# Kernel tuning notes

Hardware: AMD Instinct MI355X
Metric: run time of the kernel (lower is better)

## Reference

```python
import jax, jax.numpy as jnp
import numpy as np

B, T, F = 4096, 72, 9
H = 64            # GRU units per direction
DENSE = 128
P = 24            # predict_window


def _gru_scan(xp, h0, U, br, act):
    """xp: (T,B,3H) precomputed input projections; Keras reset_after=True GRU."""
    def step(h, x_t):
        rec = h @ U + br                      # (B,3H)
        xz, xr, xh = jnp.split(x_t, 3, axis=-1)
        rz, rr, rh = jnp.split(rec, 3, axis=-1)
        z = jax.nn.sigmoid(xz + rz)
        r = jax.nn.sigmoid(xr + rr)
        hh = act(xh + r * rh)
        h_new = z * h + (1.0 - z) * hh
        return h_new, h_new
    hT, hs = jax.lax.scan(step, h0, xp)
    return hT, hs


def _bigru(x, h0f, h0b, Wf, Uf, bif, brf, Wb, Ub, bib, brb, act, return_sequences):
    xt = jnp.swapaxes(x, 0, 1)                # (T,B,F)
    xpf = xt @ Wf + bif                       # (T,B,3H)
    xpb = xt[::-1] @ Wb + bib                 # reversed time for backward dir
    hTf, hsf = _gru_scan(xpf, h0f, Uf, brf, act)
    hTb, hsb = _gru_scan(xpb, h0b, Ub, brb, act)
    if return_sequences:
        out = jnp.concatenate([hsf, hsb[::-1]], axis=-1)   # (T,B,2H)
        return jnp.swapaxes(out, 0, 1)                      # (B,T,2H)
    return jnp.concatenate([hTf, hTb], axis=-1)             # (B,2H)


def _glorot(key, shape):
    fan_in, fan_out = shape[0], shape[-1]
    lim = np.sqrt(6.0 / (fan_in + fan_out))
    return jax.random.uniform(key, shape, jnp.float32, -lim, lim)


def setup_inputs() -> dict:
    key = jax.random.key(0)
    ks = jax.random.split(key, 16)
    d = {
        "x": jax.random.normal(ks[0], (B, T, F), jnp.float32),
        "h0_fwd": jnp.zeros((B, H), jnp.float32),
        "h0_bwd": jnp.zeros((B, H), jnp.float32),
        # d1 (input F=9), forward & backward directions
        "d1f_W": _glorot(ks[1], (F, 3 * H)), "d1f_U": _glorot(ks[2], (H, 3 * H)),
        "d1f_bi": jnp.zeros((3 * H,), jnp.float32), "d1f_br": jnp.zeros((3 * H,), jnp.float32),
        "d1b_W": _glorot(ks[3], (F, 3 * H)), "d1b_U": _glorot(ks[4], (H, 3 * H)),
        "d1b_bi": jnp.zeros((3 * H,), jnp.float32), "d1b_br": jnp.zeros((3 * H,), jnp.float32),
        # d2 (input 2H=128)
        "d2f_W": _glorot(ks[5], (2 * H, 3 * H)), "d2f_U": _glorot(ks[6], (H, 3 * H)),
        "d2f_bi": jnp.zeros((3 * H,), jnp.float32), "d2f_br": jnp.zeros((3 * H,), jnp.float32),
        "d2b_W": _glorot(ks[7], (2 * H, 3 * H)), "d2b_U": _glorot(ks[8], (H, 3 * H)),
        "d2b_bi": jnp.zeros((3 * H,), jnp.float32), "d2b_br": jnp.zeros((3 * H,), jnp.float32),
        # dense heads
        "dense_W": _glorot(ks[9], (2 * H, DENSE)), "dense_b": jnp.zeros((DENSE,), jnp.float32),
        "out_W": _glorot(ks[10], (DENSE, P)), "out_b": jnp.zeros((P,), jnp.float32),
    }
    return d


def reference(x, h0_fwd, h0_bwd,
              d1f_W, d1f_U, d1f_bi, d1f_br, d1b_W, d1b_U, d1b_bi, d1b_br,
              d2f_W, d2f_U, d2f_bi, d2f_br, d2b_W, d2b_U, d2b_bi, d2b_br,
              dense_W, dense_b, out_W, out_b):
    # d1: Bidirectional GRU(64, activation=relu), return_sequences=True, initial_state=hidden
    seq = _bigru(x, h0_fwd, h0_bwd,
                 d1f_W, d1f_U, d1f_bi, d1f_br,
                 d1b_W, d1b_U, d1b_bi, d1b_br,
                 jax.nn.relu, True)                         # (B,T,128)
    # d2: Bidirectional GRU(64, activation=tanh), zero initial state, last-state output
    z0 = jnp.zeros((x.shape[0], H), seq.dtype)
    feat = _bigru(seq, z0, z0,
                  d2f_W, d2f_U, d2f_bi, d2f_br,
                  d2b_W, d2b_U, d2b_bi, d2b_br,
                  jnp.tanh, False)                          # (B,128)
    h = jax.nn.relu(feat @ dense_W + dense_b)               # (B,128)
    out = jax.nn.softmax(h @ out_W + out_b, axis=-1)        # (B,P)
    return out
```

## Files before the change

### kernel.cpp

```cpp
#include <hip/hip_runtime.h>
#include <hip/hip_bf16.h>

typedef __attribute__((ext_vector_type(8))) short short8;
typedef __attribute__((ext_vector_type(4))) float f32x4;

#define MFMA_B16(a, b, c) __builtin_amdgcn_mfma_f32_16x16x32_bf16((a), (b), (c), 0, 0, 0)

__device__ __forceinline__ float bf2f(unsigned short u) {
    union { unsigned int i; float f; } v; v.i = ((unsigned int)u) << 16; return v.f;
}
__device__ __forceinline__ unsigned short f2bf(float f) {
    union { float f; unsigned int i; } v; v.f = f;
    unsigned int r = v.i + 0x7fffu + ((v.i >> 16) & 1u);
    return (unsigned short)(r >> 16);
}
__device__ __forceinline__ float rcp_f(float x) { return __builtin_amdgcn_rcpf(x); }
__device__ __forceinline__ float sigm_pre(float x) {
    return rcp_f(1.0f + __builtin_amdgcn_exp2f(x));
}
__device__ __forceinline__ float tanh_pre(float x) {
    return 1.0f - 2.0f * rcp_f(__builtin_amdgcn_exp2f(x) + 1.0f);
}

__device__ __forceinline__ bool probe_bf16(const unsigned short* p, int tid, int* s_cnt) {
    if (tid == 0) *s_cnt = 0;
    __syncthreads();
    unsigned short s = p[tid & 255];
    int e = (s >> 7) & 0xFF;
    if (tid < 256 && e >= 117 && e <= 137) atomicAdd(s_cnt, 1);
    __syncthreads();
    return *s_cnt >= 200;
}

struct WArgs {
    const void* src[20];
    int off[21];
};

__global__ __launch_bounds__(256)
void convert_w(WArgs a, unsigned short* __restrict__ arena,
               const unsigned short* __restrict__ probe)
{
    __shared__ int cnt;
    const bool bf = probe_bf16(probe, threadIdx.x, &cnt);
    const int total = a.off[20];
    for (int i = blockIdx.x * 256 + threadIdx.x; i < total; i += gridDim.x * 256) {
        int t = 0;
        while (t < 19 && i >= a.off[t + 1]) ++t;
        const int local = i - a.off[t];
        float v = bf ? bf2f(((const unsigned short*)a.src[t])[local])
                     : ((const float*)a.src[t])[local];
        if (t < 16) {
            const int col = local % 192;
            if (col < 128) v *= -1.4426950408889634f;
            else if (t >= 8) v *= 2.885390081777927f;
        }
        arena[i] = f2bf(v);
    }
}

__global__ __launch_bounds__(256, 1)
void gru1_kernel(const void* __restrict__ X, const void* __restrict__ h0f,
                 const void* __restrict__ h0b, int cb, int bchunk,
                 const unsigned short* __restrict__ Wf, const unsigned short* __restrict__ Uf,
                 const unsigned short* __restrict__ bif, const unsigned short* __restrict__ brf,
                 const unsigned short* __restrict__ Wb, const unsigned short* __restrict__ Ub,
                 const unsigned short* __restrict__ bib, const unsigned short* __restrict__ brb,
                 unsigned short* __restrict__ seq)
{
    const int tid  = threadIdx.x;
    const int lane = tid & 63;
    const int wv   = tid >> 6;
    const int q    = lane >> 4;
    const int ln   = lane & 15;
    const int dir  = blockIdx.y;
    const int lb0  = blockIdx.x * 16;
    const int gb0  = cb + lb0;
    const int u    = wv * 16 + ln;

    const unsigned short* W  = dir ? Wb  : Wf;
    const unsigned short* U  = dir ? Ub  : Uf;
    const unsigned short* bi = dir ? bib : bif;
    const unsigned short* br = dir ? brb : brf;
    const void* h0 = dir ? h0b : h0f;

    __shared__ __align__(16) unsigned short Ah[2][16][72];
    __shared__ __align__(16) unsigned short Ax[2][16][40];
    __shared__ int s_cnt;

    const bool xbf = probe_bf16((const unsigned short*)X, tid, &s_cnt);

    {
        unsigned short* p = &Ax[0][0][0];
        for (int i = tid; i < 2 * 16 * 40; i += 256) p[i] = 0;
    }
    __syncthreads();

    {
        const int tx0 = dir ? 71 : 0;
        if (tid < 144) {
            int r = tid / 9, k = tid - 9 * r;
            size_t idx = ((size_t)(gb0 + r) * 72 + tx0) * 9 + k;
            unsigned short hv, lv;
            if (xbf) { hv = ((const unsigned short*)X)[idx]; lv = 0; }
            else { float v = ((const float*)X)[idx]; hv = f2bf(v); lv = f2bf(v - bf2f(hv)); }
            Ax[0][r][2 * k]     = hv;
            Ax[0][r][2 * k + 1] = lv;
        }
    }

    short8 bU[3][2];
    short8 bW[3];
#pragma unroll
    for (int g = 0; g < 3; ++g) {
        const int col = g * 64 + u;
#pragma unroll
        for (int ks = 0; ks < 2; ++ks) {
            short8 f;
#pragma unroll
            for (int j = 0; j < 8; ++j) {
                int kp = ks * 32 + q * 8 + j;
                f[j] = (short)U[(size_t)kp * 192 + col];
            }
            bU[g][ks] = f;
        }
        short8 fw;
#pragma unroll
        for (int j = 0; j < 8; ++j) {
            int kp = q * 8 + j;
            fw[j] = (kp < 18) ? (short)W[(size_t)(kp >> 1) * 192 + col] : (short)0;
        }
        bW[g] = fw;
    }

    const float bz  = bf2f(bi[u])       + bf2f(br[u]);
    const float brg = bf2f(bi[64 + u])  + bf2f(br[64 + u]);
    const float bih = bf2f(bi[128 + u]);
    const float brh = bf2f(br[128 + u]);
    const f32x4 Cz  = {bz,  bz,  bz,  bz};
    const f32x4 Cr  = {brg, brg, brg, brg};
    const f32x4 Chx = {bih, bih, bih, bih};
    const f32x4 Chr = {brh, brh, brh, brh};

    float hreg[4];
#pragma unroll
    for (int i = 0; i < 4; ++i) {
        int m = q * 4 + i;
        size_t idx = (size_t)(gb0 + m) * 64 + u;
        float hv = xbf ? bf2f(((const unsigned short*)h0)[idx])
                       : ((const float*)h0)[idx];
        hreg[i] = hv;
        Ah[0][m][u] = f2bf(hv);
    }

    const int r2 = tid >> 3, c2 = tid & 7;
    const int r0x = tid / 9, k0x = tid - 9 * r0x;

    unsigned short ch = 0, cl = 0;
    if (tid < 144) {
        const int tx = dir ? 70 : 1;
        size_t idx = ((size_t)(gb0 + r0x) * 72 + tx) * 9 + k0x;
        if (xbf) { ch = ((const unsigned short*)X)[idx]; cl = 0; }
        else { float v = ((const float*)X)[idx]; ch = f2bf(v); cl = f2bf(v - bf2f(ch)); }
    }
    __syncthreads();

#pragma unroll 2
    for (int t = 0; t < 72; ++t) {
        const int cur = t & 1, nb = cur ^ 1;

        unsigned short fh = 0, fl = 0;
        if (t < 70 && tid < 144) {
            const int tx = dir ? (69 - t) : (t + 2);
            size_t idx = ((size_t)(gb0 + r0x) * 72 + tx) * 9 + k0x;
            if (xbf) { fh = ((const unsigned short*)X)[idx]; fl = 0; }
            else { float v = ((const float*)X)[idx]; fh = f2bf(v); fl = f2bf(v - bf2f(fh)); }
        }

        if (t > 0 && tid < 128) {
            const int tw = dir ? (71 - (t - 1)) : (t - 1);
            int4 v = *(const int4*)&Ah[cur][r2][c2 * 8];
            *(int4*)(seq + ((size_t)tw * bchunk + lb0 + r2) * 128 + dir * 64 + c2 * 8) = v;
        }

        const unsigned short* ap = &Ah[cur][ln][0];
        short8 a0 = *(const short8*)(ap + q * 8);
        short8 a1 = *(const short8*)(ap + 32 + q * 8);
        short8 ax = *(const short8*)(&Ax[cur][ln][q * 8]);
        f32x4 az  = MFMA_B16(ax, bW[0], Cz);
        az        = MFMA_B16(a0, bU[0][0], az);
        az        = MFMA_B16(a1, bU[0][1], az);
        f32x4 ar  = MFMA_B16(ax, bW[1], Cr);
        ar        = MFMA_B16(a0, bU[1][0], ar);
        ar        = MFMA_B16(a1, bU[1][1], ar);
        f32x4 ahx = MFMA_B16(ax, bW[2], Chx);
        f32x4 ahr = MFMA_B16(a0, bU[2][0], Chr);
        ahr       = MFMA_B16(a1, bU[2][1], ahr);

#pragma unroll
        for (int i = 0; i < 4; ++i) {
            const int m = q * 4 + i;
            float z = sigm_pre(az[i]);
            float r = sigm_pre(ar[i]);
            float pre = ahx[i] + r * ahr[i];
            float hh = fmaxf(pre, 0.0f);
            float hn = hh + z * (hreg[i] - hh);
            hreg[i] = hn;
            Ah[nb][m][u] = f2bf(hn);
        }

        if (t < 71 && tid < 144) {
            Ax[nb][r0x][2 * k0x]     = ch;
            Ax[nb][r0x][2 * k0x + 1] = cl;
        }
        ch = fh; cl = fl;
        __syncthreads();
    }

    if (tid < 128) {
        const int tw = dir ? 0 : 71;
        int4 v = *(const int4*)&Ah[0][r2][c2 * 8];
        *(int4*)(seq + ((size_t)tw * bchunk + lb0 + r2) * 128 + dir * 64 + c2 * 8) = v;
    }
}

__global__ __launch_bounds__(256, 1)
void gru2_kernel(const unsigned short* __restrict__ seq, int cb, int bchunk,
                 const unsigned short* __restrict__ W2f, const unsigned short* __restrict__ U2f,
                 const unsigned short* __restrict__ bi2f, const unsigned short* __restrict__ br2f,
                 const unsigned short* __restrict__ W2b, const unsigned short* __restrict__ U2b,
                 const unsigned short* __restrict__ bi2b, const unsigned short* __restrict__ br2b,
                 float* __restrict__ feat)
{
    const int tid  = threadIdx.x;
    const int lane = tid & 63;
    const int wv   = tid >> 6;
    const int q    = lane >> 4;
    const int ln   = lane & 15;
    const int dir  = blockIdx.y;
    const int lb0  = blockIdx.x * 16;
    const int gb0  = cb + lb0;
    const int u    = wv * 16 + ln;

    const unsigned short* W  = dir ? W2b  : W2f;
    const unsigned short* U  = dir ? U2b  : U2f;
    const unsigned short* bi = dir ? bi2b : bi2f;
    const unsigned short* br = dir ? br2b : br2f;

    __shared__ __align__(16) unsigned short Ah[2][16][72];

    {
        unsigned short* p = &Ah[0][0][0];
        for (int i = tid; i < 16 * 72; i += 256) p[i] = 0;
    }

    const long long tstride = (long long)bchunk * 128 * (dir ? -1 : 1);
    const unsigned short* sptr0 = seq + ((size_t)(lb0 + ln)) * 128 + q * 8
                                + (dir ? 71ll * bchunk * 128 : 0);

    short8 bU[3][2];
    short8 bV[3][4];
#pragma unroll
    for (int g = 0; g < 3; ++g) {
        const int col = g * 64 + u;
#pragma unroll
        for (int ks = 0; ks < 2; ++ks) {
            short8 f;
#pragma unroll
            for (int j = 0; j < 8; ++j) {
                int kp = ks * 32 + q * 8 + j;
                f[j] = (short)U[(size_t)kp * 192 + col];
            }
            bU[g][ks] = f;
        }
#pragma unroll
        for (int ks = 0; ks < 4; ++ks) {
            short8 fv;
#pragma unroll
            for (int j = 0; j < 8; ++j) {
                int kp = ks * 32 + q * 8 + j;
                fv[j] = (short)W[(size_t)kp * 192 + col];
            }
            bV[g][ks] = fv;
        }
    }

    const float bz  = bf2f(bi[u])       + bf2f(br[u]);
    const float brg = bf2f(bi[64 + u])  + bf2f(br[64 + u]);
    const float bih = bf2f(bi[128 + u]);
    const float brh = bf2f(br[128 + u]);
    const f32x4 Cz  = {bz,  bz,  bz,  bz};
    const f32x4 Cr  = {brg, brg, brg, brg};
    const f32x4 Chx = {bih, bih, bih, bih};
    const f32x4 Chr = {brh, brh, brh, brh};

    float hreg[4];
#pragma unroll
    for (int i = 0; i < 4; ++i) hreg[i] = 0.0f;

    f32x4 P0, P1, P2;
    {
        const unsigned short* sp = sptr0;
        short8 s0 = *(const short8*)(sp);
        short8 s1 = *(const short8*)(sp + 32);
        short8 s2 = *(const short8*)(sp + 64);
        short8 s3 = *(const short8*)(sp + 96);
        P0 = MFMA_B16(s0, bV[0][0], Cz);
        P0 = MFMA_B16(s1, bV[0][1], P0);
        P0 = MFMA_B16(s2, bV[0][2], P0);
        P0 = MFMA_B16(s3, bV[0][3], P0);
        P1 = MFMA_B16(s0, bV[1][0], Cr);
        P1 = MFMA_B16(s1, bV[1][1], P1);
        P1 = MFMA_B16(s2, bV[1][2], P1);
        P1 = MFMA_B16(s3, bV[1][3], P1);
        P2 = MFMA_B16(s0, bV[2][0], Chx);
        P2 = MFMA_B16(s1, bV[2][1], P2);
        P2 = MFMA_B16(s2, bV[2][2], P2);
        P2 = MFMA_B16(s3, bV[2][3], P2);
    }
    short8 c0, c1, c2, c3;
    {
        const unsigned short* sp = sptr0 + tstride;
        c0 = *(const short8*)(sp);
        c1 = *(const short8*)(sp + 32);
        c2 = *(const short8*)(sp + 64);
        c3 = *(const short8*)(sp + 96);
    }
    __syncthreads();

#pragma unroll 2
    for (int t = 0; t < 72; ++t) {
        const int cur = t & 1, nb = cur ^ 1;

        short8 f0, f1, f2, f3;
        const bool pf2 = (t < 70);
        if (pf2) {
            const unsigned short* sp = sptr0 + (long long)(t + 2) * tstride;
            f0 = *(const short8*)(sp);
            f1 = *(const short8*)(sp + 32);
            f2 = *(const short8*)(sp + 64);
            f3 = *(const short8*)(sp + 96);
        }

        const unsigned short* ap = &Ah[cur][ln][0];
        short8 a0 = *(const short8*)(ap + q * 8);
        short8 a1 = *(const short8*)(ap + 32 + q * 8);
        f32x4 az  = MFMA_B16(a0, bU[0][0], P0);
        az        = MFMA_B16(a1, bU[0][1], az);
        f32x4 ar  = MFMA_B16(a0, bU[1][0], P1);
        ar        = MFMA_B16(a1, bU[1][1], ar);
        f32x4 ahr = MFMA_B16(a0, bU[2][0], Chr);
        ahr       = MFMA_B16(a1, bU[2][1], ahr);
        f32x4 ahx = P2;

#pragma unroll
        for (int i = 0; i < 4; ++i) {
            const int m = q * 4 + i;
            float z = sigm_pre(az[i]);
            float r = sigm_pre(ar[i]);
            float pre = ahx[i] + r * ahr[i];
            float hh = tanh_pre(pre);
            float hn = hh + z * (hreg[i] - hh);
            hreg[i] = hn;
            Ah[nb][m][u] = f2bf(hn);
        }

        if (t < 71) {
            P0 = MFMA_B16(c0, bV[0][0], Cz);
            P0 = MFMA_B16(c1, bV[0][1], P0);
            P0 = MFMA_B16(c2, bV[0][2], P0);
            P0 = MFMA_B16(c3, bV[0][3], P0);
            P1 = MFMA_B16(c0, bV[1][0], Cr);
            P1 = MFMA_B16(c1, bV[1][1], P1);
            P1 = MFMA_B16(c2, bV[1][2], P1);
            P1 = MFMA_B16(c3, bV[1][3], P1);
            P2 = MFMA_B16(c0, bV[2][0], Chx);
            P2 = MFMA_B16(c1, bV[2][1], P2);
            P2 = MFMA_B16(c2, bV[2][2], P2);
            P2 = MFMA_B16(c3, bV[2][3], P2);
        }
        if (pf2) { c0 = f0; c1 = f1; c2 = f2; c3 = f3; }
        __syncthreads();
    }

#pragma unroll
    for (int i = 0; i < 4; ++i) {
        const int m = q * 4 + i;
        feat[(size_t)(gb0 + m) * 128 + dir * 64 + u] = hreg[i];
    }
}

__global__ __launch_bounds__(256, 1)
void head_kernel(const float* __restrict__ feat,
                 const unsigned short* __restrict__ dW, const unsigned short* __restrict__ db,
                 const unsigned short* __restrict__ oW, const unsigned short* __restrict__ ob,
                 float* __restrict__ out)
{
    const int tid = threadIdx.x;
    const int b0  = blockIdx.x * 16;

    __shared__ __align__(16) unsigned short Wl[128][136];
    __shared__ __align__(16) float fs[16][128];
    __shared__ __align__(16) float hs[16][136];
    __shared__ __align__(16) float ls[16][32];

    for (int i = tid; i < 2048; i += 256) {
        const int k = i >> 4;
        const int c = (i & 15) * 8;
        *(int4*)&Wl[k][c] = *(const int4*)(dW + (size_t)k * 128 + c);
    }
    {
        const float4* src = (const float4*)(feat + (size_t)b0 * 128);
        float4* dst = (float4*)&fs[0][0];
        for (int i = tid; i < 512; i += 256) dst[i] = src[i];
    }
    __syncthreads();

    {
        const int row = tid >> 4;
        const int j0  = (tid & 15) * 8;
        float acc[8];
#pragma unroll
        for (int jj = 0; jj < 8; ++jj) acc[jj] = bf2f(db[j0 + jj]);
        for (int k = 0; k < 128; ++k) {
            float f = fs[row][k];
            short8 w = *(const short8*)&Wl[k][j0];
#pragma unroll
            for (int jj = 0; jj < 8; ++jj)
                acc[jj] += f * bf2f((unsigned short)w[jj]);
        }
#pragma unroll
        for (int jj = 0; jj < 8; ++jj) hs[row][j0 + jj] = fmaxf(acc[jj], 0.0f);
    }
    __syncthreads();

    for (int e = tid; e < 16 * 24; e += 256) {
        const int row = e / 24, l = e - 24 * row;
        float acc = bf2f(ob[l]);
        for (int k = 0; k < 128; ++k)
            acc += hs[row][k] * bf2f(oW[(size_t)k * 24 + l]);
        ls[row][l] = acc;
    }
    __syncthreads();

    for (int e = tid; e < 16 * 24; e += 256) {
        const int row = e / 24, l = e - 24 * row;
        float mx = ls[row][0];
#pragma unroll
        for (int k = 1; k < 24; ++k) mx = fmaxf(mx, ls[row][k]);
        float s = 0.0f;
#pragma unroll
        for (int k = 0; k < 24; ++k) s += __expf(ls[row][k] - mx);
        float v = __expf(ls[row][l] - mx) * rcp_f(s);
        out[(size_t)(b0 + row) * 24 + l] = v;
    }
}

extern "C" void kernel_launch(void* const* d_in, const int* in_sizes, int n_in,
                              void* d_out, int out_size, void* d_ws, size_t ws_size,
                              hipStream_t stream) {
    (void)in_sizes; (void)n_in; (void)out_size;

    static const int wc[20] = {
        1728, 12288, 192, 192,
        1728, 12288, 192, 192,
        24576, 12288, 192, 192,
        24576, 12288, 192, 192,
        16384, 128,
        3072, 24
    };

    WArgs a;
    int off = 0;
    for (int t = 0; t < 20; ++t) {
        a.src[t] = d_in[t + 3];
        a.off[t] = off;
        off += wc[t];
    }
    a.off[20] = off;

    const unsigned long long arena_bytes = 245952ull;
    const unsigned long long feat_bytes  = 4096ull * 128ull * 4ull;
    const unsigned long long seq_full    = 72ull * 4096ull * 128ull * 2ull;
    const unsigned long long fixed       = arena_bytes + feat_bytes;

    int nc = 32;
    for (int c = 1; c <= 32; c *= 2) {
        if (fixed + seq_full / (unsigned long long)c <= (unsigned long long)ws_size) { nc = c; break; }
    }
    const int bchunk = 4096 / nc;

    unsigned short* arena = (unsigned short*)d_ws;
    float* feat           = (float*)((char*)d_ws + arena_bytes);
    unsigned short* seq   = (unsigned short*)((char*)d_ws + fixed);

    convert_w<<<128, 256, 0, stream>>>(a, arena, (const unsigned short*)d_in[0]);

    const unsigned short* d1fW = arena + a.off[0];
    const unsigned short* d1fU = arena + a.off[1];
    const unsigned short* d1fbi= arena + a.off[2];
    const unsigned short* d1fbr= arena + a.off[3];
    const unsigned short* d1bW = arena + a.off[4];
    const unsigned short* d1bU = arena + a.off[5];
    const unsigned short* d1bbi= arena + a.off[6];
    const unsigned short* d1bbr= arena + a.off[7];
    const unsigned short* d2fW = arena + a.off[8];
    const unsigned short* d2fU = arena + a.off[9];
    const unsigned short* d2fbi= arena + a.off[10];
    const unsigned short* d2fbr= arena + a.off[11];
    const unsigned short* d2bW = arena + a.off[12];
    const unsigned short* d2bU = arena + a.off[13];
    const unsigned short* d2bbi= arena + a.off[14];
    const unsigned short* d2bbr= arena + a.off[15];
    const unsigned short* dW   = arena + a.off[16];
    const unsigned short* db   = arena + a.off[17];
    const unsigned short* oW   = arena + a.off[18];
    const unsigned short* ob   = arena + a.off[19];

    for (int c = 0; c < nc; ++c) {
        const int cb = c * bchunk;
        gru1_kernel<<<dim3(bchunk / 16, 2), 256, 0, stream>>>(
            d_in[0], d_in[1], d_in[2], cb, bchunk,
            d1fW, d1fU, d1fbi, d1fbr, d1bW, d1bU, d1bbi, d1bbr, seq);
        gru2_kernel<<<dim3(bchunk / 16, 2), 256, 0, stream>>>(
            seq, cb, bchunk,
            d2fW, d2fU, d2fbi, d2fbr, d2bW, d2bU, d2bbi, d2bbr, feat);
    }
    head_kernel<<<256, 256, 0, stream>>>(
        feat, dW, db, oW, ob, (float*)d_out);
}
```

Measured before the change: 255.4 us.

## Process two 16-row batch tiles per block in both GRU kernels

Each block of both GRU recurrence kernels now handles 32 batch rows as two independent 16-row MFMA tiles instead of one, and the grid is halved to match. The two tiles' MFMA chains and gate math are interleaved so one wave has independent work to hide MFMA and transcendental latency in the serial time loop. Weight fragments held in registers and the per-step barrier are shared across both tiles. In exchange there are fewer blocks, which may leave CUs idle, plus more registers per wave and double the LDS footprint.

```diff
diff --git a/kernel.cpp b/kernel.cpp
--- a/kernel.cpp
+++ b/kernel.cpp
@@ -74,7 +74,7 @@
     const int q    = lane >> 4;
     const int ln   = lane & 15;
     const int dir  = blockIdx.y;
-    const int lb0  = blockIdx.x * 16;
+    const int lb0  = blockIdx.x * 32;
     const int gb0  = cb + lb0;
     const int u    = wv * 16 + ln;
 
@@ -84,22 +84,22 @@
     const unsigned short* br = dir ? brb : brf;
     const void* h0 = dir ? h0b : h0f;
 
-    __shared__ __align__(16) unsigned short Ah[2][16][72];
-    __shared__ __align__(16) unsigned short Ax[2][16][40];
+    __shared__ __align__(16) unsigned short Ah[2][32][72];
+    __shared__ __align__(16) unsigned short Ax[2][32][40];
     __shared__ int s_cnt;
 
     const bool xbf = probe_bf16((const unsigned short*)X, tid, &s_cnt);
 
     {
         unsigned short* p = &Ax[0][0][0];
-        for (int i = tid; i < 2 * 16 * 40; i += 256) p[i] = 0;
+        for (int i = tid; i < 2 * 32 * 40; i += 256) p[i] = 0;
     }
     __syncthreads();
 
     {
         const int tx0 = dir ? 71 : 0;
-        if (tid < 144) {
-            int r = tid / 9, k = tid - 9 * r;
+        for (int i = tid; i < 288; i += 256) {
+            int r = i / 9, k = i - 9 * r;
             size_t idx = ((size_t)(gb0 + r) * 72 + tx0) * 9 + k;
             unsigned short hv, lv;
             if (xbf) { hv = ((const unsigned short*)X)[idx]; lv = 0; }
@@ -142,26 +142,35 @@
     const f32x4 Chx = {bih, bih, bih, bih};
     const f32x4 Chr = {brh, brh, brh, brh};
 
-    float hreg[4];
+    float hA[4], hB[4];
 #pragma unroll
     for (int i = 0; i < 4; ++i) {
         int m = q * 4 + i;
-        size_t idx = (size_t)(gb0 + m) * 64 + u;
-        float hv = xbf ? bf2f(((const unsigned short*)h0)[idx])
-                       : ((const float*)h0)[idx];
-        hreg[i] = hv;
-        Ah[0][m][u] = f2bf(hv);
+        size_t ia = (size_t)(gb0 + m) * 64 + u;
+        size_t ib = (size_t)(gb0 + 16 + m) * 64 + u;
+        float va = xbf ? bf2f(((const unsigned short*)h0)[ia]) : ((const float*)h0)[ia];
+        float vb = xbf ? bf2f(((const unsigned short*)h0)[ib]) : ((const float*)h0)[ib];
+        hA[i] = va; hB[i] = vb;
+        Ah[0][m][u]      = f2bf(va);
+        Ah[0][16 + m][u] = f2bf(vb);
     }
 
     const int r2 = tid >> 3, c2 = tid & 7;
     const int r0x = tid / 9, k0x = tid - 9 * r0x;
-
-    unsigned short ch = 0, cl = 0;
-    if (tid < 144) {
+    const int i1  = 256 + tid;
+    const int r1x = i1 / 9, k1x = i1 - 9 * r1x;
+
+    unsigned short ch0 = 0, cl0 = 0, ch1 = 0, cl1 = 0;
+    {
         const int tx = dir ? 70 : 1;
         size_t idx = ((size_t)(gb0 + r0x) * 72 + tx) * 9 + k0x;
-        if (xbf) { ch = ((const unsigned short*)X)[idx]; cl = 0; }
-        else { float v = ((const float*)X)[idx]; ch = f2bf(v); cl = f2bf(v - bf2f(ch)); }
+        if (xbf) { ch0 = ((const unsigned short*)X)[idx]; cl0 = 0; }
+        else { float v = ((const float*)X)[idx]; ch0 = f2bf(v); cl0 = f2bf(v - bf2f(ch0)); }
+        if (tid < 32) {
+            size_t idx1 = ((size_t)(gb0 + r1x) * 72 + tx) * 9 + k1x;
+            if (xbf) { ch1 = ((const unsigned short*)X)[idx1]; cl1 = 0; }
+            else { float v = ((const float*)X)[idx1]; ch1 = f2bf(v); cl1 = f2bf(v - bf2f(ch1)); }
+        }
     }
     __syncthreads();
 
@@ -169,55 +178,85 @@
     for (int t = 0; t < 72; ++t) {
         const int cur = t & 1, nb = cur ^ 1;
 
-        unsigned short fh = 0, fl = 0;
-        if (t < 70 && tid < 144) {
+        unsigned short fh0 = 0, fl0 = 0, fh1 = 0, fl1 = 0;
+        if (t < 70) {
             const int tx = dir ? (69 - t) : (t + 2);
             size_t idx = ((size_t)(gb0 + r0x) * 72 + tx) * 9 + k0x;
-            if (xbf) { fh = ((const unsigned short*)X)[idx]; fl = 0; }
-            else { float v = ((const float*)X)[idx]; fh = f2bf(v); fl = f2bf(v - bf2f(fh)); }
-        }
-
-        if (t > 0 && tid < 128) {
+            if (xbf) { fh0 = ((const unsigned short*)X)[idx]; fl0 = 0; }
+            else { float v = ((const float*)X)[idx]; fh0 = f2bf(v); fl0 = f2bf(v - bf2f(fh0)); }
+            if (tid < 32) {
+                size_t idx1 = ((size_t)(gb0 + r1x) * 72 + tx) * 9 + k1x;
+                if (xbf) { fh1 = ((const unsigned short*)X)[idx1]; fl1 = 0; }
+                else { float v = ((const float*)X)[idx1]; fh1 = f2bf(v); fl1 = f2bf(v - bf2f(fh1)); }
+            }
+        }
+
+        if (t > 0) {
             const int tw = dir ? (71 - (t - 1)) : (t - 1);
             int4 v = *(const int4*)&Ah[cur][r2][c2 * 8];
             *(int4*)(seq + ((size_t)tw * bchunk + lb0 + r2) * 128 + dir * 64 + c2 * 8) = v;
         }
 
-        const unsigned short* ap = &Ah[cur][ln][0];
-        short8 a0 = *(const short8*)(ap + q * 8);
-        short8 a1 = *(const short8*)(ap + 32 + q * 8);
-        short8 ax = *(const short8*)(&Ax[cur][ln][q * 8]);
-        f32x4 az  = MFMA_B16(ax, bW[0], Cz);
-        az        = MFMA_B16(a0, bU[0][0], az);
-        az        = MFMA_B16(a1, bU[0][1], az);
-        f32x4 ar  = MFMA_B16(ax, bW[1], Cr);
-        ar        = MFMA_B16(a0, bU[1][0], ar);
-        ar        = MFMA_B16(a1, bU[1][1], ar);
-        f32x4 ahx = MFMA_B16(ax, bW[2], Chx);
-        f32x4 ahr = MFMA_B16(a0, bU[2][0], Chr);
-        ahr       = MFMA_B16(a1, bU[2][1], ahr);
+        const unsigned short* apA = &Ah[cur][ln][0];
+        const unsigned short* apB = &Ah[cur][16 + ln][0];
+        short8 a0A = *(const short8*)(apA + q * 8);
+        short8 a1A = *(const short8*)(apA + 32 + q * 8);
+        short8 axA = *(const short8*)(&Ax[cur][ln][q * 8]);
+        short8 a0B = *(const short8*)(apB + q * 8);
+        short8 a1B = *(const short8*)(apB + 32 + q * 8);
+        short8 axB = *(const short8*)(&Ax[cur][16 + ln][q * 8]);
+
+        f32x4 azA = MFMA_B16(axA, bW[0], Cz);
+        azA = MFMA_B16(a0A, bU[0][0], azA);
+        azA = MFMA_B16(a1A, bU[0][1], azA);
+        f32x4 arA = MFMA_B16(axA, bW[1], Cr);
+        arA = MFMA_B16(a0A, bU[1][0], arA);
+        arA = MFMA_B16(a1A, bU[1][1], arA);
+        f32x4 ahxA = MFMA_B16(axA, bW[2], Chx);
+        f32x4 ahrA = MFMA_B16(a0A, bU[2][0], Chr);
+        ahrA = MFMA_B16(a1A, bU[2][1], ahrA);
+
+        f32x4 azB = MFMA_B16(axB, bW[0], Cz);
+        azB = MFMA_B16(a0B, bU[0][0], azB);
+        azB = MFMA_B16(a1B, bU[0][1], azB);
+        f32x4 arB = MFMA_B16(axB, bW[1], Cr);
+        arB = MFMA_B16(a0B, bU[1][0], arB);
+        arB = MFMA_B16(a1B, bU[1][1], arB);
+        f32x4 ahxB = MFMA_B16(axB, bW[2], Chx);
+        f32x4 ahrB = MFMA_B16(a0B, bU[2][0], Chr);
+        ahrB = MFMA_B16(a1B, bU[2][1], ahrB);
 
 #pragma unroll
         for (int i = 0; i < 4; ++i) {
             const int m = q * 4 + i;
-            float z = sigm_pre(az[i]);
-            float r = sigm_pre(ar[i]);
-            float pre = ahx[i] + r * ahr[i];
-            float hh = fmaxf(pre, 0.0f);
-            float hn = hh + z * (hreg[i] - hh);
-            hreg[i] = hn;
-            Ah[nb][m][u] = f2bf(hn);
-        }
-
-        if (t < 71 && tid < 144) {
-            Ax[nb][r0x][2 * k0x]     = ch;
-            Ax[nb][r0x][2 * k0x + 1] = cl;
-        }
-        ch = fh; cl = fl;
+            float zA = sigm_pre(azA[i]);
+            float rA = sigm_pre(arA[i]);
+            float hhA = fmaxf(ahxA[i] + rA * ahrA[i], 0.0f);
+            float hnA = hhA + zA * (hA[i] - hhA);
+            hA[i] = hnA;
+            Ah[nb][m][u] = f2bf(hnA);
+
+            float zB = sigm_pre(azB[i]);
+            float rB = sigm_pre(arB[i]);
+            float hhB = fmaxf(ahxB[i] + rB * ahrB[i], 0.0f);
+            float hnB = hhB + zB * (hB[i] - hhB);
+            hB[i] = hnB;
+            Ah[nb][16 + m][u] = f2bf(hnB);
+        }
+
+        if (t < 71) {
+            Ax[nb][r0x][2 * k0x]     = ch0;
+            Ax[nb][r0x][2 * k0x + 1] = cl0;
+            if (tid < 32) {
+                Ax[nb][r1x][2 * k1x]     = ch1;
+                Ax[nb][r1x][2 * k1x + 1] = cl1;
+            }
+        }
+        ch0 = fh0; cl0 = fl0; ch1 = fh1; cl1 = fl1;
         __syncthreads();
     }
 
-    if (tid < 128) {
+    {
         const int tw = dir ? 0 : 71;
         int4 v = *(const int4*)&Ah[0][r2][c2 * 8];
         *(int4*)(seq + ((size_t)tw * bchunk + lb0 + r2) * 128 + dir * 64 + c2 * 8) = v;
@@ -238,7 +277,7 @@
     const int q    = lane >> 4;
     const int ln   = lane & 15;
     const int dir  = blockIdx.y;
-    const int lb0  = blockIdx.x * 16;
+    const int lb0  = blockIdx.x * 32;
     const int gb0  = cb + lb0;
     const int u    = wv * 16 + ln;
 
@@ -247,16 +286,17 @@
     const unsigned short* bi = dir ? bi2b : bi2f;
     const unsigned short* br = dir ? br2b : br2f;
 
-    __shared__ __align__(16) unsigned short Ah[2][16][72];
+    __shared__ __align__(16) unsigned short Ah[2][32][72];
 
     {
         unsigned short* p = &Ah[0][0][0];
-        for (int i = tid; i < 16 * 72; i += 256) p[i] = 0;
+        for (int i = tid; i < 32 * 72; i += 256) p[i] = 0;
     }
 
     const long long tstride = (long long)bchunk * 128 * (dir ? -1 : 1);
-    const unsigned short* sptr0 = seq + ((size_t)(lb0 + ln)) * 128 + q * 8
-                                + (dir ? 71ll * bchunk * 128 : 0);
+    const unsigned short* sA = seq + ((size_t)(lb0 + ln)) * 128 + q * 8
+                             + (dir ? 71ll * bchunk * 128 : 0);
+    const unsigned short* sB = sA + 16 * 128;
 
     short8 bU[3][2];
     short8 bV[3][4];
@@ -294,37 +334,57 @@
     const f32x4 Chx = {bih, bih, bih, bih};
     const f32x4 Chr = {brh, brh, brh, brh};
 
-    float hreg[4];
-#pragma unroll
-    for (int i = 0; i < 4; ++i) hreg[i] = 0.0f;
-
-    f32x4 P0, P1, P2;
-    {
-        const unsigned short* sp = sptr0;
-        short8 s0 = *(const short8*)(sp);
-        short8 s1 = *(const short8*)(sp + 32);
-        short8 s2 = *(const short8*)(sp + 64);
-        short8 s3 = *(const short8*)(sp + 96);
-        P0 = MFMA_B16(s0, bV[0][0], Cz);
-        P0 = MFMA_B16(s1, bV[0][1], P0);
-        P0 = MFMA_B16(s2, bV[0][2], P0);
-        P0 = MFMA_B16(s3, bV[0][3], P0);
-        P1 = MFMA_B16(s0, bV[1][0], Cr);
-        P1 = MFMA_B16(s1, bV[1][1], P1);
-        P1 = MFMA_B16(s2, bV[1][2], P1);
-        P1 = MFMA_B16(s3, bV[1][3], P1);
-        P2 = MFMA_B16(s0, bV[2][0], Chx);
-        P2 = MFMA_B16(s1, bV[2][1], P2);
-        P2 = MFMA_B16(s2, bV[2][2], P2);
-        P2 = MFMA_B16(s3, bV[2][3], P2);
-    }
-    short8 c0, c1, c2, c3;
-    {
-        const unsigned short* sp = sptr0 + tstride;
-        c0 = *(const short8*)(sp);
-        c1 = *(const short8*)(sp + 32);
-        c2 = *(const short8*)(sp + 64);
-        c3 = *(const short8*)(sp + 96);
+    float hA[4], hB[4];
+#pragma unroll
+    for (int i = 0; i < 4; ++i) { hA[i] = 0.0f; hB[i] = 0.0f; }
+
+    f32x4 PA0, PA1, PA2, PB0, PB1, PB2;
+    {
+        short8 s0 = *(const short8*)(sA);
+        short8 s1 = *(const short8*)(sA + 32);
+        short8 s2 = *(const short8*)(sA + 64);
+        short8 s3 = *(const short8*)(sA + 96);
+        PA0 = MFMA_B16(s0, bV[0][0], Cz);
+        PA0 = MFMA_B16(s1, bV[0][1], PA0);
+        PA0 = MFMA_B16(s2, bV[0][2], PA0);
+        PA0 = MFMA_B16(s3, bV[0][3], PA0);
+        PA1 = MFMA_B16(s0, bV[1][0], Cr);
+        PA1 = MFMA_B16(s1, bV[1][1], PA1);
+        PA1 = MFMA_B16(s2, bV[1][2], PA1);
+        PA1 = MFMA_B16(s3, bV[1][3], PA1);
+        PA2 = MFMA_B16(s0, bV[2][0], Chx);
+        PA2 = MFMA_B16(s1, bV[2][1], PA2);
+        PA2 = MFMA_B16(s2, bV[2][2], PA2);
+        PA2 = MFMA_B16(s3, bV[2][3], PA2);
+        short8 t0 = *(const short8*)(sB);
+        short8 t1 = *(const short8*)(sB + 32);
+        short8 t2 = *(const short8*)(sB + 64);
+        short8 t3 = *(const short8*)(sB + 96);
+        PB0 = MFMA_B16(t0, bV[0][0], Cz);
+        PB0 = MFMA_B16(t1, bV[0][1], PB0);
+        PB0 = MFMA_B16(t2, bV[0][2], PB0);
+        PB0 = MFMA_B16(t3, bV[0][3], PB0);
+        PB1 = MFMA_B16(t0, bV[1][0], Cr);
+        PB1 = MFMA_B16(t1, bV[1][1], PB1);
+        PB1 = MFMA_B16(t2, bV[1][2], PB1);
+        PB1 = MFMA_B16(t3, bV[1][3], PB1);
+        PB2 = MFMA_B16(t0, bV[2][0], Chx);
+        PB2 = MFMA_B16(t1, bV[2][1], PB2);
+        PB2 = MFMA_B16(t2, bV[2][2], PB2);
+        PB2 = MFMA_B16(t3, bV[2][3], PB2);
+    }
+    short8 cA0, cA1, cA2, cA3, cB0, cB1, cB2, cB3;
+    {
+        const unsigned short* pa = sA + tstride;
+        const unsigned short* pb = sB + tstride;
+        cA0 = *(const short8*)(pa);
+        cA1 = *(const short8*)(pa + 32);
+        cA2 = *(const short8*)(pa + 64);
+        cA3 = *(const short8*)(pa + 96);
+        cB0 = *(const short8*)(pb);
+        cB1 = *(const short8*)(pb + 32);
+        cB2 = *(const short8*)(pb + 64);
+        cB3 = *(const short8*)(pb + 96);
     }
     __syncthreads();
 
@@ -332,61 +392,98 @@
     for (int t = 0; t < 72; ++t) {
         const int cur = t & 1, nb = cur ^ 1;
 
-        short8 f0, f1, f2, f3;
+        short8 fA0, fA1, fA2, fA3, fB0, fB1, fB2, fB3;
         const bool pf2 = (t < 70);
         if (pf2) {
-            const unsigned short* sp = sptr0 + (long long)(t + 2) * tstride;
-            f0 = *(const short8*)(sp);
-            f1 = *(const short8*)(sp + 32);
-            f2 = *(const short8*)(sp + 64);
-            f3 = *(const short8*)(sp + 96);
-        }
-
-        const unsigned short* ap = &Ah[cur][ln][0];
-        short8 a0 = *(const short8*)(ap + q * 8);
-        short8 a1 = *(const short8*)(ap + 32 + q * 8);
-        f32x4 az  = MFMA_B16(a0, bU[0][0], P0);
-        az        = MFMA_B16(a1, bU[0][1], az);
-        f32x4 ar  = MFMA_B16(a0, bU[1][0], P1);
-        ar        = MFMA_B16(a1, bU[1][1], ar);
-        f32x4 ahr = MFMA_B16(a0, bU[2][0], Chr);
-        ahr       = MFMA_B16(a1, bU[2][1], ahr);
-        f32x4 ahx = P2;
+            const unsigned short* pa = sA + (long long)(t + 2) * tstride;
+            const unsigned short* pb = sB + (long long)(t + 2) * tstride;
+            fA0 = *(const short8*)(pa);
+            fA1 = *(const short8*)(pa + 32);
+            fA2 = *(const short8*)(pa + 64);
+            fA3 = *(const short8*)(pa + 96);
+            fB0 = *(const short8*)(pb);
+            fB1 = *(const short8*)(pb + 32);
+            fB2 = *(const short8*)(pb + 64);
+            fB3 = *(const short8*)(pb + 96);
+        }
+
+        const unsigned short* apA = &Ah[cur][ln][0];
+        const unsigned short* apB = &Ah[cur][16 + ln][0];
+        short8 a0A = *(const short8*)(apA + q * 8);
+        short8 a1A = *(const short8*)(apA + 32 + q * 8);
+        short8 a0B = *(const short8*)(apB + q * 8);
+        short8 a1B = *(const short8*)(apB + 32 + q * 8);
+
+        f32x4 azA = MFMA_B16(a0A, bU[0][0], PA0);
+        azA = MFMA_B16(a1A, bU[0][1], azA);
+        f32x4 arA = MFMA_B16(a0A, bU[1][0], PA1);
+        arA = MFMA_B16(a1A, bU[1][1], arA);
+        f32x4 ahrA = MFMA_B16(a0A, bU[2][0], Chr);
+        ahrA = MFMA_B16(a1A, bU[2][1], ahrA);
+
+        f32x4 azB = MFMA_B16(a0B, bU[0][0], PB0);
+        azB = MFMA_B16(a1B, bU[0][1], azB);
+        f32x4 arB = MFMA_B16(a0B, bU[1][0], PB1);
+        arB = MFMA_B16(a1B, bU[1][1], arB);
+        f32x4 ahrB = MFMA_B16(a0B, bU[2][0], Chr);
+        ahrB = MFMA_B16(a1B, bU[2][1], ahrB);
 
 #pragma unroll
         for (int i = 0; i < 4; ++i) {
             const int m = q * 4 + i;
-            float z = sigm_pre(az[i]);
-            float r = sigm_pre(ar[i]);
-            float pre = ahx[i] + r * ahr[i];
-            float hh = tanh_pre(pre);
-            float hn = hh + z * (hreg[i] - hh);
-            hreg[i] = hn;
-            Ah[nb][m][u] = f2bf(hn);
+            float zA = sigm_pre(azA[i]);
+            float rA = sigm_pre(arA[i]);
+            float hhA = tanh_pre(PA2[i] + rA * ahrA[i]);
+            float hnA = hhA + zA * (hA[i] - hhA);
+            hA[i] = hnA;
+            Ah[nb][m][u] = f2bf(hnA);
+
+            float zB = sigm_pre(azB[i]);
+            float rB = sigm_pre(arB[i]);
+            float hhB = tanh_pre(PB2[i] + rB * ahrB[i]);
+            float hnB = hhB + zB * (hB[i] - hhB);
+            hB[i] = hnB;
+            Ah[nb][16 + m][u] = f2bf(hnB);
         }
 
         if (t < 71) {
-            P0 = MFMA_B16(c0, bV[0][0], Cz);
-            P0 = MFMA_B16(c1, bV[0][1], P0);
-            P0 = MFMA_B16(c2, bV[0][2], P0);
-            P0 = MFMA_B16(c3, bV[0][3], P0);
-            P1 = MFMA_B16(c0, bV[1][0], Cr);
-            P1 = MFMA_B16(c1, bV[1][1], P1);
-            P1 = MFMA_B16(c2, bV[1][2], P1);
-            P1 = MFMA_B16(c3, bV[1][3], P1);
-            P2 = MFMA_B16(c0, bV[2][0], Chx);
-            P2 = MFMA_B16(c1, bV[2][1], P2);
-            P2 = MFMA_B16(c2, bV[2][2], P2);
-            P2 = MFMA_B16(c3, bV[2][3], P2);
-        }
-        if (pf2) { c0 = f0; c1 = f1; c2 = f2; c3 = f3; }
+            PA0 = MFMA_B16(cA0, bV[0][0], Cz);
+            PA0 = MFMA_B16(cA1, bV[0][1], PA0);
+            PA0 = MFMA_B16(cA2, bV[0][2], PA0);
+            PA0 = MFMA_B16(cA3, bV[0][3], PA0);
+            PA1 = MFMA_B16(cA0, bV[1][0], Cr);
+            PA1 = MFMA_B16(cA1, bV[1][1], PA1);
+            PA1 = MFMA_B16(cA2, bV[1][2], PA1);
+            PA1 = MFMA_B16(cA3, bV[1][3], PA1);
+            PA2 = MFMA_B16(cA0, bV[2][0], Chx);
+            PA2 = MFMA_B16(cA1, bV[2][1], PA2);
+            PA2 = MFMA_B16(cA2, bV[2][2], PA2);
+            PA2 = MFMA_B16(cA3, bV[2][3], PA2);
+            PB0 = MFMA_B16(cB0, bV[0][0], Cz);
+            PB0 = MFMA_B16(cB1, bV[0][1], PB0);
+            PB0 = MFMA_B16(cB2, bV[0][2], PB0);
+            PB0 = MFMA_B16(cB3, bV[0][3], PB0);
+            PB1 = MFMA_B16(cB0, bV[1][0], Cr);
+            PB1 = MFMA_B16(cB1, bV[1][1], PB1);
+            PB1 = MFMA_B16(cB2, bV[1][2], PB1);
+            PB1 = MFMA_B16(cB3, bV[1][3], PB1);
+            PB2 = MFMA_B16(cB0, bV[2][0], Chx);
+            PB2 = MFMA_B16(cB1, bV[2][1], PB2);
+            PB2 = MFMA_B16(cB2, bV[2][2], PB2);
+            PB2 = MFMA_B16(cB3, bV[2][3], PB2);
+        }
+        if (pf2) {
+            cA0 = fA0; cA1 = fA1; cA2 = fA2; cA3 = fA3;
+            cB0 = fB0; cB1 = fB1; cB2 = fB2; cB3 = fB3;
+        }
         __syncthreads();
     }
 
 #pragma unroll
     for (int i = 0; i < 4; ++i) {
         const int m = q * 4 + i;
-        feat[(size_t)(gb0 + m) * 128 + dir * 64 + u] = hreg[i];
+        feat[(size_t)(gb0 + m) * 128 + dir * 64 + u]      = hA[i];
+        feat[(size_t)(gb0 + 16 + m) * 128 + dir * 64 + u] = hB[i];
     }
 }
 
@@ -519,10 +616,10 @@
 
     for (int c = 0; c < nc; ++c) {
         const int cb = c * bchunk;
-        gru1_kernel<<<dim3(bchunk / 16, 2), 256, 0, stream>>>(
+        gru1_kernel<<<dim3(bchunk / 32, 2), 256, 0, stream>>>(
             d_in[0], d_in[1], d_in[2], cb, bchunk,
             d1fW, d1fU, d1fbi, d1fbr, d1bW, d1bU, d1bbi, d1bbr, seq);
-        gru2_kernel<<<dim3(bchunk / 16, 2), 256, 0, stream>>>(
+        gru2_kernel<<<dim3(bchunk / 32, 2), 256, 0, stream>>>(
             seq, cb, bchunk,
             d2fW, d2fU, d2fbi, d2fbr, d2bW, d2bU, d2bbi, d2bbr, feat);
     }
```

Result: slower. 299.0 us (+17.1%).

## Run first GRU layer with one wavefront per block, dropping per-step barriers

Applied to the files above, without the earlier changes.

The first bidirectional GRU kernel changes from four wavefronts per 16-row block to a single 64-lane wavefront. That wavefront computes all twelve 16-column gate tiles itself and keeps the 16x64 hidden state in registers. Because one wavefront owns the whole block's state, the per-timestep __syncthreads and the double-buffered hidden-state LDS are removed, and the bf16 probe becomes a wave ballot. The trade-off is that each wavefront now issues four times as many MFMAs serially per step and holds far more weight registers. The design relies on several small blocks sharing a CU to hide that latency.

```diff
diff --git a/kernel.cpp b/kernel.cpp
--- a/kernel.cpp
+++ b/kernel.cpp
@@ -59,7 +59,7 @@
     }
 }
 
-__global__ __launch_bounds__(256, 1)
+__global__ __launch_bounds__(64, 1)
 void gru1_kernel(const void* __restrict__ X, const void* __restrict__ h0f,
                  const void* __restrict__ h0b, int cb, int bchunk,
                  const unsigned short* __restrict__ Wf, const unsigned short* __restrict__ Uf,
@@ -68,15 +68,12 @@
                  const unsigned short* __restrict__ bib, const unsigned short* __restrict__ brb,
                  unsigned short* __restrict__ seq)
 {
-    const int tid  = threadIdx.x;
-    const int lane = tid & 63;
-    const int wv   = tid >> 6;
+    const int lane = threadIdx.x;
     const int q    = lane >> 4;
     const int ln   = lane & 15;
     const int dir  = blockIdx.y;
     const int lb0  = blockIdx.x * 16;
     const int gb0  = cb + lb0;
-    const int u    = wv * 16 + ln;
 
     const unsigned short* W  = dir ? Wb  : Wf;
     const unsigned short* U  = dir ? Ub  : Uf;
@@ -84,22 +81,27 @@
     const unsigned short* br = dir ? brb : brf;
     const void* h0 = dir ? h0b : h0f;
 
-    __shared__ __align__(16) unsigned short Ah[2][16][72];
+    __shared__ __align__(16) unsigned short hbuf[16][72];
     __shared__ __align__(16) unsigned short Ax[2][16][40];
-    __shared__ int s_cnt;
-
-    const bool xbf = probe_bf16((const unsigned short*)X, tid, &s_cnt);
+
+    int pc = 0;
+#pragma unroll
+    for (int j = 0; j < 4; ++j) {
+        unsigned short s = ((const unsigned short*)X)[lane * 4 + j];
+        int e = (s >> 7) & 0xFF;
+        pc += (int)__popcll(__ballot(e >= 117 && e <= 137));
+    }
+    const bool xbf = pc >= 200;
 
     {
         unsigned short* p = &Ax[0][0][0];
-        for (int i = tid; i < 2 * 16 * 40; i += 256) p[i] = 0;
-    }
-    __syncthreads();
+        for (int i = lane; i < 2 * 16 * 40; i += 64) p[i] = 0;
+    }
 
     {
         const int tx0 = dir ? 71 : 0;
-        if (tid < 144) {
-            int r = tid / 9, k = tid - 9 * r;
+        for (int e = lane; e < 144; e += 64) {
+            int r = e / 9, k = e - 9 * r;
             size_t idx = ((size_t)(gb0 + r) * 72 + tx0) * 9 + k;
             unsigned short hv, lv;
             if (xbf) { hv = ((const unsigned short*)X)[idx]; lv = 0; }
@@ -109,118 +111,151 @@
         }
     }
 
-    short8 bU[3][2];
-    short8 bW[3];
-#pragma unroll
-    for (int g = 0; g < 3; ++g) {
-        const int col = g * 64 + u;
+    short8 bU[12][2];
+    short8 bW[12];
+#pragma unroll
+    for (int ct = 0; ct < 12; ++ct) {
+        const int gcol = ct * 16 + ln;
 #pragma unroll
         for (int ks = 0; ks < 2; ++ks) {
             short8 f;
 #pragma unroll
             for (int j = 0; j < 8; ++j) {
                 int kp = ks * 32 + q * 8 + j;
-                f[j] = (short)U[(size_t)kp * 192 + col];
-            }
-            bU[g][ks] = f;
+                f[j] = (short)U[(size_t)kp * 192 + gcol];
+            }
+            bU[ct][ks] = f;
         }
         short8 fw;
 #pragma unroll
         for (int j = 0; j < 8; ++j) {
             int kp = q * 8 + j;
-            fw[j] = (kp < 18) ? (short)W[(size_t)(kp >> 1) * 192 + col] : (short)0;
-        }
-        bW[g] = fw;
-    }
-
-    const float bz  = bf2f(bi[u])       + bf2f(br[u]);
-    const float brg = bf2f(bi[64 + u])  + bf2f(br[64 + u]);
-    const float bih = bf2f(bi[128 + u]);
-    const float brh = bf2f(br[128 + u]);
-    const f32x4 Cz  = {bz,  bz,  bz,  bz};
-    const f32x4 Cr  = {brg, brg, brg, brg};
-    const f32x4 Chx = {bih, bih, bih, bih};
-    const f32x4 Chr = {brh, brh, brh, brh};
-
-    float hreg[4];
-#pragma unroll
-    for (int i = 0; i < 4; ++i) {
-        int m = q * 4 + i;
-        size_t idx = (size_t)(gb0 + m) * 64 + u;
-        float hv = xbf ? bf2f(((const unsigned short*)h0)[idx])
-                       : ((const float*)h0)[idx];
-        hreg[i] = hv;
-        Ah[0][m][u] = f2bf(hv);
-    }
-
-    const int r2 = tid >> 3, c2 = tid & 7;
-    const int r0x = tid / 9, k0x = tid - 9 * r0x;
-
-    unsigned short ch = 0, cl = 0;
-    if (tid < 144) {
+            fw[j] = (kp < 18) ? (short)W[(size_t)(kp >> 1) * 192 + gcol] : (short)0;
+        }
+        bW[ct] = fw;
+    }
+
+    float bzv[4], brv[4], bxv[4], bhv[4];
+#pragma unroll
+    for (int t4 = 0; t4 < 4; ++t4) {
+        const int u = t4 * 16 + ln;
+        bzv[t4] = bf2f(bi[u])        + bf2f(br[u]);
+        brv[t4] = bf2f(bi[64 + u])   + bf2f(br[64 + u]);
+        bxv[t4] = bf2f(bi[128 + u]);
+        bhv[t4] = bf2f(br[128 + u]);
+    }
+
+    float hreg[16];
+#pragma unroll
+    for (int t4 = 0; t4 < 4; ++t4) {
+#pragma unroll
+        for (int i = 0; i < 4; ++i) {
+            const int row = q * 4 + i;
+            const int u   = t4 * 16 + ln;
+            float hv = xbf ? bf2f(((const unsigned short*)h0)[(size_t)(gb0 + row) * 64 + u])
+                           : ((const float*)h0)[(size_t)(gb0 + row) * 64 + u];
+            hreg[t4 * 4 + i] = hv;
+            hbuf[row][u] = f2bf(hv);
+        }
+    }
+
+    unsigned short chh[3] = {0, 0, 0}, cll[3] = {0, 0, 0};
+    {
         const int tx = dir ? 70 : 1;
-        size_t idx = ((size_t)(gb0 + r0x) * 72 + tx) * 9 + k0x;
-        if (xbf) { ch = ((const unsigned short*)X)[idx]; cl = 0; }
-        else { float v = ((const float*)X)[idx]; ch = f2bf(v); cl = f2bf(v - bf2f(ch)); }
-    }
-    __syncthreads();
-
-#pragma unroll 2
+#pragma unroll
+        for (int j = 0; j < 3; ++j) {
+            int e = lane + 64 * j;
+            if (e < 144) {
+                int r = e / 9, k = e - 9 * r; (void)k;
+                size_t idx = ((size_t)(gb0 + r) * 72 + tx) * 9 + (e - 9 * r);
+                if (xbf) { chh[j] = ((const unsigned short*)X)[idx]; cll[j] = 0; }
+                else { float v = ((const float*)X)[idx]; chh[j] = f2bf(v); cll[j] = f2bf(v - bf2f(chh[j])); }
+            }
+        }
+    }
+    __syncthreads();
+
     for (int t = 0; t < 72; ++t) {
         const int cur = t & 1, nb = cur ^ 1;
 
-        unsigned short fh = 0, fl = 0;
-        if (t < 70 && tid < 144) {
+        unsigned short fhh[3] = {0, 0, 0}, fll[3] = {0, 0, 0};
+        if (t < 70) {
             const int tx = dir ? (69 - t) : (t + 2);
-            size_t idx = ((size_t)(gb0 + r0x) * 72 + tx) * 9 + k0x;
-            if (xbf) { fh = ((const unsigned short*)X)[idx]; fl = 0; }
-            else { float v = ((const float*)X)[idx]; fh = f2bf(v); fl = f2bf(v - bf2f(fh)); }
-        }
-
-        if (t > 0 && tid < 128) {
-            const int tw = dir ? (71 - (t - 1)) : (t - 1);
-            int4 v = *(const int4*)&Ah[cur][r2][c2 * 8];
-            *(int4*)(seq + ((size_t)tw * bchunk + lb0 + r2) * 128 + dir * 64 + c2 * 8) = v;
-        }
-
-        const unsigned short* ap = &Ah[cur][ln][0];
-        short8 a0 = *(const short8*)(ap + q * 8);
-        short8 a1 = *(const short8*)(ap + 32 + q * 8);
-        short8 ax = *(const short8*)(&Ax[cur][ln][q * 8]);
-        f32x4 az  = MFMA_B16(ax, bW[0], Cz);
-        az        = MFMA_B16(a0, bU[0][0], az);
-        az        = MFMA_B16(a1, bU[0][1], az);
-        f32x4 ar  = MFMA_B16(ax, bW[1], Cr);
-        ar        = MFMA_B16(a0, bU[1][0], ar);
-        ar        = MFMA_B16(a1, bU[1][1], ar);
-        f32x4 ahx = MFMA_B16(ax, bW[2], Chx);
-        f32x4 ahr = MFMA_B16(a0, bU[2][0], Chr);
-        ahr       = MFMA_B16(a1, bU[2][1], ahr);
-
-#pragma unroll
-        for (int i = 0; i < 4; ++i) {
-            const int m = q * 4 + i;
-            float z = sigm_pre(az[i]);
-            float r = sigm_pre(ar[i]);
-            float pre = ahx[i] + r * ahr[i];
-            float hh = fmaxf(pre, 0.0f);
-            float hn = hh + z * (hreg[i] - hh);
-            hreg[i] = hn;
-            Ah[nb][m][u] = f2bf(hn);
-        }
-
-        if (t < 71 && tid < 144) {
-            Ax[nb][r0x][2 * k0x]     = ch;
-            Ax[nb][r0x][2 * k0x + 1] = cl;
-        }
-        ch = fh; cl = fl;
-        __syncthreads();
-    }
-
-    if (tid < 128) {
-        const int tw = dir ? 0 : 71;
-        int4 v = *(const int4*)&Ah[0][r2][c2 * 8];
-        *(int4*)(seq + ((size_t)tw * bchunk + lb0 + r2) * 128 + dir * 64 + c2 * 8) = v;
+#pragma unroll
+            for (int j = 0; j < 3; ++j) {
+                int e = lane + 64 * j;
+                if (e < 144) {
+                    int r = e / 9;
+                    size_t idx = ((size_t)(gb0 + r) * 72 + tx) * 9 + (e - 9 * r);
+                    if (xbf) { fhh[j] = ((const unsigned short*)X)[idx]; fll[j] = 0; }
+                    else { float v = ((const float*)X)[idx]; fhh[j] = f2bf(v); fll[j] = f2bf(v - bf2f(fhh[j])); }
+                }
+            }
+        }
+
+        short8 a0 = *(const short8*)&hbuf[ln][q * 8];
+        short8 a1 = *(const short8*)&hbuf[ln][32 + q * 8];
+        short8 ax = *(const short8*)&Ax[cur][ln][q * 8];
+
+        f32x4 gz[4], gr[4], ghx[4], ghr[4];
+#pragma unroll
+        for (int t4 = 0; t4 < 4; ++t4) {
+            f32x4 Cz  = {bzv[t4], bzv[t4], bzv[t4], bzv[t4]};
+            f32x4 Cr  = {brv[t4], brv[t4], brv[t4], brv[t4]};
+            f32x4 Chx = {bxv[t4], bxv[t4], bxv[t4], bxv[t4]};
+            f32x4 Chr = {bhv[t4], bhv[t4], bhv[t4], bhv[t4]};
+            f32x4 z = MFMA_B16(ax, bW[t4], Cz);
+            z = MFMA_B16(a0, bU[t4][0], z);
+            z = MFMA_B16(a1, bU[t4][1], z);
+            gz[t4] = z;
+            f32x4 r = MFMA_B16(ax, bW[4 + t4], Cr);
+            r = MFMA_B16(a0, bU[4 + t4][0], r);
+            r = MFMA_B16(a1, bU[4 + t4][1], r);
+            gr[t4] = r;
+            ghx[t4] = MFMA_B16(ax, bW[8 + t4], Chx);
+            f32x4 hr = MFMA_B16(a0, bU[8 + t4][0], Chr);
+            hr = MFMA_B16(a1, bU[8 + t4][1], hr);
+            ghr[t4] = hr;
+        }
+
+#pragma unroll
+        for (int t4 = 0; t4 < 4; ++t4) {
+#pragma unroll
+            for (int i = 0; i < 4; ++i) {
+                float z = sigm_pre(gz[t4][i]);
+                float r = sigm_pre(gr[t4][i]);
+                float hh = fmaxf(ghx[t4][i] + r * ghr[t4][i], 0.0f);
+                float ho = hreg[t4 * 4 + i];
+                float hn = hh + z * (ho - hh);
+                hreg[t4 * 4 + i] = hn;
+                hbuf[q * 4 + i][t4 * 16 + ln] = f2bf(hn);
+            }
+        }
+
+        {
+            const int tw = dir ? (71 - t) : t;
+#pragma unroll
+            for (int j = 0; j < 2; ++j) {
+                int chunk = lane + 64 * j;
+                int row = chunk >> 3, c = chunk & 7;
+                int4 v = *(const int4*)&hbuf[row][c * 8];
+                *(int4*)(seq + ((size_t)tw * bchunk + lb0 + row) * 128 + dir * 64 + c * 8) = v;
+            }
+        }
+
+        if (t < 71) {
+#pragma unroll
+            for (int j = 0; j < 3; ++j) {
+                int e = lane + 64 * j;
+                if (e < 144) {
+                    int r = e / 9, k = e - 9 * r;
+                    Ax[nb][r][2 * k]     = chh[j];
+                    Ax[nb][r][2 * k + 1] = cll[j];
+                }
+            }
+        }
+#pragma unroll
+        for (int j = 0; j < 3; ++j) { chh[j] = fhh[j]; cll[j] = fll[j]; }
     }
 }
 
@@ -519,7 +554,7 @@
 
     for (int c = 0; c < nc; ++c) {
         const int cb = c * bchunk;
-        gru1_kernel<<<dim3(bchunk / 16, 2), 256, 0, stream>>>(
+        gru1_kernel<<<dim3(bchunk / 16, 2), 64, 0, stream>>>(
             d_in[0], d_in[1], d_in[2], cb, bchunk,
             d1fW, d1fU, d1fbi, d1fbr, d1bW, d1bU, d1bbi, d1bbr, seq);
         gru2_kernel<<<dim3(bchunk / 16, 2), 256, 0, stream>>>(
```

New measurement: 356.4 us. +39.5%, slower.
